# Performance work log

Hardware: AMD Instinct MI355X
Metric: run time of the kernel (lower is better)

## Reference

```python
import jax, jax.numpy as jnp
import numpy as np

OUT_H, OUT_W = 224, 224  # output_size init kwarg


def setup_inputs() -> dict:
    key = jax.random.key(0)
    k1, k2 = jax.random.split(key)
    B, H, W, C = 16, 384, 384, 64
    X = jax.random.normal(k1, (B, H, W, C), dtype=jnp.float32)
    # near-identity 3x3 projective transforms (row-major, flattened to 9)
    eye = jnp.tile(jnp.eye(3, dtype=jnp.float32).reshape(1, 9), (B, 1))
    transformation = eye + 0.05 * jax.random.normal(k2, (B, 9), dtype=jnp.float32)
    return {"X": X, "transformation": transformation}


def reference(X, transformation):
    B, Hin, Win, C = X.shape
    N = OUT_H * OUT_W
    T = transformation.reshape(B, 3, 3)

    # regular grid in [-1,1]^2 with homogeneous coordinate
    xs = jnp.linspace(-1.0, 1.0, OUT_W)
    ys = jnp.linspace(-1.0, 1.0, OUT_H)
    xc, yc = jnp.meshgrid(xs, ys)  # (OUT_H, OUT_W)
    grid = jnp.stack([xc.ravel(), yc.ravel(), jnp.ones(N, dtype=jnp.float32)], 0)  # (3, N)

    sg = jnp.einsum('bij,jn->bin', T, grid)  # (B, 3, N)
    z = sg[:, 2] + 1e-6
    x = sg[:, 0] / z
    y = sg[:, 1] / z
    # map [-1,1] -> pixel coords (note: scaled by W/H, not W-1/H-1, as in source)
    x = 0.5 * (x + 1.0) * Win
    y = 0.5 * (y + 1.0) * Hin

    # truncation toward zero, matching tf.cast float->int32
    x0 = x.astype(jnp.int32)
    x1 = x0 + 1
    y0 = y.astype(jnp.int32)
    y1 = y0 + 1
    x0 = jnp.clip(x0, 0, Win - 1)
    x1 = jnp.clip(x1, 0, Win - 1)
    y0 = jnp.clip(y0, 0, Hin - 1)
    y1 = jnp.clip(y1, 0, Hin - 1)

    flat = X.reshape(B, Hin * Win, C)

    def gather(yy, xx):
        idx = (yy * Win + xx)[:, :, None]  # (B, N, 1)
        return jnp.take_along_axis(flat, idx, axis=1)  # (B, N, C)

    pa = gather(y0, x0)
    pb = gather(y1, x0)
    pc = gather(y0, x1)
    pd = gather(y1, x1)

    x0f = x0.astype(jnp.float32)
    x1f = x1.astype(jnp.float32)
    y0f = y0.astype(jnp.float32)
    y1f = y1.astype(jnp.float32)

    wa = ((x1f - x) * (y1f - y))[:, :, None]
    wb = ((x1f - x) * (y - y0f))[:, :, None]
    wc = ((x - x0f) * (y1f - y))[:, :, None]
    wd = ((x - x0f) * (y - y0f))[:, :, None]

    out = wa * pa + wb * pb + wc * pc + wd * pd  # (B, N, C)
    return out.reshape(B, OUT_H, OUT_W, C)
```

## Files before the change

kernel.cpp:

```cpp
#include <hip/hip_runtime.h>

#define BATCH  16
#define HIN    384
#define WIN    384
#define CH     64
#define OUTH   224
#define OUTW   224

#define PIX_PER_BLOCK 16
#define BLOCKS_PER_IMG ((OUTH * OUTW) / PIX_PER_BLOCK)
#define TOTAL_BLOCKS   (BATCH * BLOCKS_PER_IMG)
#define NXCD 8
#define BLOCKS_PER_XCD (TOTAL_BLOCKS / NXCD)

typedef float f32x4 __attribute__((ext_vector_type(4)));

__global__ __launch_bounds__(256) void bilinear_proj_kernel(
    const float* __restrict__ X,
    const float* __restrict__ Tm,
    float* __restrict__ out)
{
    const int lane       = threadIdx.x & 15;
    const int pixInBlock = threadIdx.x >> 4;

    const int lb = (blockIdx.x % NXCD) * BLOCKS_PER_XCD + blockIdx.x / NXCD;

    const int b          = lb / BLOCKS_PER_IMG;
    const int blkInImg   = lb % BLOCKS_PER_IMG;
    const int pInImg     = blkInImg * PIX_PER_BLOCK + pixInBlock;
    const int oy         = pInImg / OUTW;
    const int ox         = pInImg % OUTW;

    const float xc = -1.0f + (float)ox * (2.0f / (float)(OUTW - 1));
    const float yc = -1.0f + (float)oy * (2.0f / (float)(OUTH - 1));

    const float* t = Tm + b * 9;
    const float t0 = t[0], t1 = t[1], t2 = t[2];
    const float t3 = t[3], t4 = t[4], t5 = t[5];
    const float t6 = t[6], t7 = t[7], t8 = t[8];

    const float s0 = t0 * xc + t1 * yc + t2;
    const float s1 = t3 * xc + t4 * yc + t5;
    const float s2 = t6 * xc + t7 * yc + t8;
    const float z  = s2 + 1e-6f;
    float x = s0 / z;
    float y = s1 / z;
    x = 0.5f * (x + 1.0f) * (float)WIN;
    y = 0.5f * (y + 1.0f) * (float)HIN;

    int x0 = (int)x;
    int x1 = x0 + 1;
    int y0 = (int)y;
    int y1 = y0 + 1;
    x0 = min(max(x0, 0), WIN - 1);
    x1 = min(max(x1, 0), WIN - 1);
    y0 = min(max(y0, 0), HIN - 1);
    y1 = min(max(y1, 0), HIN - 1);

    const float x0f = (float)x0, x1f = (float)x1;
    const float y0f = (float)y0, y1f = (float)y1;
    const float wa = (x1f - x) * (y1f - y);
    const float wb = (x1f - x) * (y - y0f);
    const float wc = (x - x0f) * (y1f - y);
    const float wd = (x - x0f) * (y - y0f);

    const int c = lane * 4;
    const size_t imgBase = (size_t)b * (size_t)(HIN * WIN) * CH;

    const f32x4* pa = (const f32x4*)(X + imgBase + ((size_t)(y0 * WIN + x0)) * CH + c);
    const f32x4* pb = (const f32x4*)(X + imgBase + ((size_t)(y1 * WIN + x0)) * CH + c);
    const f32x4* pc = (const f32x4*)(X + imgBase + ((size_t)(y0 * WIN + x1)) * CH + c);
    const f32x4* pd = (const f32x4*)(X + imgBase + ((size_t)(y1 * WIN + x1)) * CH + c);

    const f32x4 va = *pa;
    const f32x4 vb = *pb;
    const f32x4 vc = *pc;
    const f32x4 vd = *pd;

    f32x4 o = wa * va + wb * vb + wc * vc + wd * vd;

    f32x4* po = (f32x4*)(out + ((size_t)b * (OUTH * OUTW) + (size_t)pInImg) * CH + c);
    __builtin_nontemporal_store(o, po);
}

extern "C" void kernel_launch(void* const* d_in, const int* in_sizes, int n_in,
                              void* d_out, int out_size, void* d_ws, size_t ws_size,
                              hipStream_t stream) {
    const float* X  = (const float*)d_in[0];
    const float* Tm = (const float*)d_in[1];
    float* out      = (float*)d_out;

    const int nblocks = TOTAL_BLOCKS;
    bilinear_proj_kernel<<<nblocks, 256, 0, stream>>>(X, Tm, out);
}
```

Baseline: 801.4 us.

## Process 2x2 pixel quads over multi-tile blocks to batch gathers and improve locality

Each block now handles four 2-row by 32-column output tiles, and each thread computes four output pixels arranged 2x2. All 16 gathers for those pixels are issued before any blending, which raises memory-level parallelism, and neighbouring output pixels share source cache lines within a block. The change cuts the block count by 16x and adds a launch-bounds occupancy hint. In exchange it uses more registers per thread and leaves fewer blocks to spread across the GPU.

```diff
diff --git a/kernel.cpp b/kernel.cpp
--- a/kernel.cpp
+++ b/kernel.cpp
@@ -7,80 +7,111 @@
 #define OUTH   224
 #define OUTW   224
 
-#define PIX_PER_BLOCK 16
-#define BLOCKS_PER_IMG ((OUTH * OUTW) / PIX_PER_BLOCK)
-#define TOTAL_BLOCKS   (BATCH * BLOCKS_PER_IMG)
+#define TILE_COLS 32
+#define COLTILES  (OUTW / TILE_COLS)
+#define ROWPAIRS  (OUTH / 2)
+#define TILES_PER_IMG (COLTILES * ROWPAIRS)
+#define TILES_PER_BLOCK 4
+#define BLOCKS_PER_IMG (TILES_PER_IMG / TILES_PER_BLOCK)
+#define TOTAL_BLOCKS (BATCH * BLOCKS_PER_IMG)
 #define NXCD 8
 #define BLOCKS_PER_XCD (TOTAL_BLOCKS / NXCD)
 
 typedef float f32x4 __attribute__((ext_vector_type(4)));
 
-__global__ __launch_bounds__(256) void bilinear_proj_kernel(
+__global__ __launch_bounds__(256, 3) void bilinear_proj_kernel(
     const float* __restrict__ X,
     const float* __restrict__ Tm,
     float* __restrict__ out)
 {
-    const int lane       = threadIdx.x & 15;
-    const int pixInBlock = threadIdx.x >> 4;
+    const int lane = threadIdx.x & 15;
+    const int slot = threadIdx.x >> 4;
 
     const int lb = (blockIdx.x % NXCD) * BLOCKS_PER_XCD + blockIdx.x / NXCD;
 
-    const int b          = lb / BLOCKS_PER_IMG;
-    const int blkInImg   = lb % BLOCKS_PER_IMG;
-    const int pInImg     = blkInImg * PIX_PER_BLOCK + pixInBlock;
-    const int oy         = pInImg / OUTW;
-    const int ox         = pInImg % OUTW;
-
-    const float xc = -1.0f + (float)ox * (2.0f / (float)(OUTW - 1));
-    const float yc = -1.0f + (float)oy * (2.0f / (float)(OUTH - 1));
+    const int b        = lb / BLOCKS_PER_IMG;
+    const int blkInImg = lb % BLOCKS_PER_IMG;
 
     const float* t = Tm + b * 9;
     const float t0 = t[0], t1 = t[1], t2 = t[2];
     const float t3 = t[3], t4 = t[4], t5 = t[5];
     const float t6 = t[6], t7 = t[7], t8 = t[8];
 
-    const float s0 = t0 * xc + t1 * yc + t2;
-    const float s1 = t3 * xc + t4 * yc + t5;
-    const float s2 = t6 * xc + t7 * yc + t8;
-    const float z  = s2 + 1e-6f;
-    float x = s0 / z;
-    float y = s1 / z;
-    x = 0.5f * (x + 1.0f) * (float)WIN;
-    y = 0.5f * (y + 1.0f) * (float)HIN;
+    const int c = lane * 4;
+    const float* Xb   = X + (size_t)b * (size_t)(HIN * WIN) * CH + c;
+    float*       outB = out + (size_t)b * (size_t)(OUTH * OUTW) * CH + c;
 
-    int x0 = (int)x;
-    int x1 = x0 + 1;
-    int y0 = (int)y;
-    int y1 = y0 + 1;
-    x0 = min(max(x0, 0), WIN - 1);
-    x1 = min(max(x1, 0), WIN - 1);
-    y0 = min(max(y0, 0), HIN - 1);
-    y1 = min(max(y1, 0), HIN - 1);
+    for (int i = 0; i < TILES_PER_BLOCK; ++i) {
+        const int tile   = blkInImg * TILES_PER_BLOCK + i;
+        const int r      = tile / COLTILES;
+        const int cIdx   = tile - r * COLTILES;
+        const int oyBase = r * 2;
+        const int ox0    = cIdx * TILE_COLS;
 
-    const float x0f = (float)x0, x1f = (float)x1;
-    const float y0f = (float)y0, y1f = (float)y1;
-    const float wa = (x1f - x) * (y1f - y);
-    const float wb = (x1f - x) * (y - y0f);
-    const float wc = (x - x0f) * (y1f - y);
-    const float wd = (x - x0f) * (y - y0f);
+        float wa[4], wb[4], wc[4], wd[4];
+        const f32x4* pa[4];
+        const f32x4* pb[4];
+        const f32x4* pc[4];
+        const f32x4* pd[4];
+        f32x4* po[4];
 
-    const int c = lane * 4;
-    const size_t imgBase = (size_t)b * (size_t)(HIN * WIN) * CH;
+        #pragma unroll
+        for (int k = 0; k < 4; ++k) {
+            const int py = k >> 1;
+            const int px = k & 1;
+            const int oy = oyBase + py;
+            const int ox = ox0 + slot + px * 16;
 
-    const f32x4* pa = (const f32x4*)(X + imgBase + ((size_t)(y0 * WIN + x0)) * CH + c);
-    const f32x4* pb = (const f32x4*)(X + imgBase + ((size_t)(y1 * WIN + x0)) * CH + c);
-    const f32x4* pc = (const f32x4*)(X + imgBase + ((size_t)(y0 * WIN + x1)) * CH + c);
-    const f32x4* pd = (const f32x4*)(X + imgBase + ((size_t)(y1 * WIN + x1)) * CH + c);
+            const float xc = -1.0f + (float)ox * (2.0f / (float)(OUTW - 1));
+            const float yc = -1.0f + (float)oy * (2.0f / (float)(OUTH - 1));
 
-    const f32x4 va = *pa;
-    const f32x4 vb = *pb;
-    const f32x4 vc = *pc;
-    const f32x4 vd = *pd;
+            const float s0 = t0 * xc + t1 * yc + t2;
+            const float s1 = t3 * xc + t4 * yc + t5;
+            const float s2 = t6 * xc + t7 * yc + t8;
+            const float z  = s2 + 1e-6f;
+            float x = s0 / z;
+            float y = s1 / z;
+            x = 0.5f * (x + 1.0f) * (float)WIN;
+            y = 0.5f * (y + 1.0f) * (float)HIN;
 
-    f32x4 o = wa * va + wb * vb + wc * vc + wd * vd;
+            int x0 = (int)x;
+            int x1 = x0 + 1;
+            int y0 = (int)y;
+            int y1 = y0 + 1;
+            x0 = min(max(x0, 0), WIN - 1);
+            x1 = min(max(x1, 0), WIN - 1);
+            y0 = min(max(y0, 0), HIN - 1);
+            y1 = min(max(y1, 0), HIN - 1);
 
-    f32x4* po = (f32x4*)(out + ((size_t)b * (OUTH * OUTW) + (size_t)pInImg) * CH + c);
-    __builtin_nontemporal_store(o, po);
+            const float x0f = (float)x0, x1f = (float)x1;
+            const float y0f = (float)y0, y1f = (float)y1;
+            wa[k] = (x1f - x) * (y1f - y);
+            wb[k] = (x1f - x) * (y - y0f);
+            wc[k] = (x - x0f) * (y1f - y);
+            wd[k] = (x - x0f) * (y - y0f);
+
+            pa[k] = (const f32x4*)(Xb + (size_t)(y0 * WIN + x0) * CH);
+            pb[k] = (const f32x4*)(Xb + (size_t)(y1 * WIN + x0) * CH);
+            pc[k] = (const f32x4*)(Xb + (size_t)(y0 * WIN + x1) * CH);
+            pd[k] = (const f32x4*)(Xb + (size_t)(y1 * WIN + x1) * CH);
+            po[k] = (f32x4*)(outB + (size_t)(oy * OUTW + ox) * CH);
+        }
+
+        f32x4 va[4], vb[4], vc[4], vd[4];
+        #pragma unroll
+        for (int k = 0; k < 4; ++k) {
+            va[k] = *pa[k];
+            vb[k] = *pb[k];
+            vc[k] = *pc[k];
+            vd[k] = *pd[k];
+        }
+
+        #pragma unroll
+        for (int k = 0; k < 4; ++k) {
+            f32x4 o = wa[k] * va[k] + wb[k] * vb[k] + wc[k] * vc[k] + wd[k] * vd[k];
+            __builtin_nontemporal_store(o, po[k]);
+        }
+    }
 }
 
 extern "C" void kernel_launch(void* const* d_in, const int* in_sizes, int n_in,
@@ -90,6 +121,5 @@
     const float* Tm = (const float*)d_in[1];
     float* out      = (float*)d_out;
 
-    const int nblocks = TOTAL_BLOCKS;
-    bilinear_proj_kernel<<<nblocks, 256, 0, stream>>>(X, Tm, out);
+    bilinear_proj_kernel<<<TOTAL_BLOCKS, 256, 0, stream>>>(X, Tm, out);
 }
```

New measurement: 827.1 us. 3.2% more time.
